# Kernel tuning notes

Hardware: AMD Instinct MI355X
Metric: run time of the kernel (lower is better)

The kernel has to match this reference:

```python
import jax, jax.numpy as jnp
import numpy as np

BS, DIM, EMB_DIM, SRC, TDEC, NEMB = 64, 512, 512, 400, 100, 50257


def intra_attention(h_t, h, W_attn):
    # h_t: [bs, dim]; h: [n, bs, dim]; W_attn: [dim, dim]
    n, bs, dim = h.shape
    # Faithful to torch .view([bs, dim, n]) on a contiguous [n, bs, dim]
    # tensor: raw row-major memory reinterpretation (NOT a transpose).
    hv = jnp.reshape(h, (bs, dim, n))  # [bs, dim, n]
    # E_t = (h_t @ W) [bs,1,dim] bmm hv [bs,dim,n] -> [bs, n]
    E = jnp.einsum('bd,bdn->bn', h_t @ W_attn, hv)
    # sum-normalized (non-softmax) score, eq. (4)
    A = E / jnp.sum(E, axis=1, keepdims=True)  # [bs, n]
    C = jnp.einsum('bdn,bn->bd', hv, A)        # [bs, dim]
    return A, C


def pointer_generator(ae_t, ce_t, hd_t, cd_t, W_emb, W_proj, W_u, b_u, b_out):
    # c_cat: [3*dim, bs]
    c_cat = jnp.concatenate((hd_t, ce_t, cd_t), axis=1).T
    # p_switch: [bs]
    p_switch = jax.nn.sigmoid(W_u @ c_cat + b_u).squeeze(0)
    # shared-embedding output projection, sect 2.4
    W_out = jnp.tanh(W_emb @ W_proj)           # [n_emb, 3*dim]
    logits = W_out @ c_cat + b_out             # [n_emb, bs]
    p_vocab = jax.nn.softmax(logits, axis=0)   # softmax over vocab
    p_gen = ((1.0 - p_switch) * p_vocab).T     # [bs, n_emb]
    p_copy = p_switch[:, None] * ae_t          # [bs, src]
    return p_gen, p_copy


def setup_inputs() -> dict:
    key = jax.random.key(0)
    ks = jax.random.split(key, 12)
    inp = {
        'h_t': jax.random.uniform(ks[0], (BS, DIM), dtype=jnp.float32),
        'h_enc': jax.random.uniform(ks[1], (SRC, BS, DIM), dtype=jnp.float32),
        'h_dec': jax.random.uniform(ks[2], (TDEC, BS, DIM), dtype=jnp.float32),
        'x': jax.random.randint(ks[3], (SRC, BS, 1), 0, NEMB, dtype=jnp.int64) if jax.config.jax_enable_x64 else jax.random.randint(ks[3], (SRC, BS, 1), 0, NEMB, dtype=jnp.int32),
        # positive attention weights keep the sum-normalized score well-conditioned
        'W_attn_enc': jax.random.uniform(ks[4], (DIM, DIM), dtype=jnp.float32, maxval=0.05),
        'W_attn_dec': jax.random.uniform(ks[5], (DIM, DIM), dtype=jnp.float32, maxval=0.05),
        'W_emb': jax.random.normal(ks[6], (NEMB, EMB_DIM), dtype=jnp.float32) * 0.02,
        'W_proj': jax.random.normal(ks[7], (EMB_DIM, 3 * DIM), dtype=jnp.float32) * 0.02,
        'W_u': jax.random.normal(ks[8], (1, 3 * DIM), dtype=jnp.float32) * 0.02,
        'b_u': jnp.zeros((1,), dtype=jnp.float32),
        'b_out': jnp.zeros((NEMB, 1), dtype=jnp.float32),
    }
    return inp


def reference(h_t, h_enc, h_dec, x, W_attn_enc, W_attn_dec, W_emb, W_proj, W_u, b_u, b_out):
    # one decode step of ReinforcedDecoder: enc attn + dec attn + pointer-gen
    ae_t, ce_t = intra_attention(h_t, h_enc, W_attn_enc)
    ad_t, cd_t = intra_attention(h_t, h_dec, W_attn_dec)
    p_gen, p_copy = pointer_generator(ae_t, ce_t, h_t, cd_t,
                                      W_emb, W_proj, W_u, b_u, b_out)
    return p_gen, p_copy
```

## Files before the change

kernel.cpp:

```cpp
#include <hip/hip_runtime.h>
#include <math.h>

typedef __attribute__((ext_vector_type(8))) short bf16x8;
typedef __attribute__((ext_vector_type(4))) float f32x4;
typedef __attribute__((ext_vector_type(4))) float f4v;

#define BS   64
#define DIM  512
#define SRC  400
#define TDEC 100
#define NEMB 50257
#define K3   1536

#define WS_Q     0
#define WS_EENC  65536
#define WS_EDEC  91136
#define WS_CENC  97536
#define WS_CDEC  130304
#define WS_ESUM  163072
#define WS_PSW   163200
#define WS_SMAX  163264
#define WS_SSUM  163328
#define WS_WPT   163392
#define WS_CCB   556608
#define WS_ZBEG  WS_CENC
#define WS_ZCNT  (WS_WPT - WS_CENC)

__device__ __forceinline__ ushort f2bf(float x) {
    union { float f; unsigned u; } v; v.f = x;
    unsigned r = (v.u + 0x7FFFu + ((v.u >> 16) & 1u)) >> 16;
    return (ushort)r;
}
__device__ __forceinline__ bf16x8 pack8v(f4v a, f4v b) {
    union { ushort us[8]; bf16x8 v; } p;
    p.us[0] = f2bf(a.x); p.us[1] = f2bf(a.y); p.us[2] = f2bf(a.z); p.us[3] = f2bf(a.w);
    p.us[4] = f2bf(b.x); p.us[5] = f2bf(b.y); p.us[6] = f2bf(b.z); p.us[7] = f2bf(b.w);
    return p.v;
}
__device__ __forceinline__ float pade_tanh(float x) {
    const float x2 = x * x;
    const float num = x * fmaf(x2, 1.0f / 15.0f, 1.0f);
    const float den = fmaf(x2, 0.4f, 1.0f);
    return num * __frcp_rn(den);
}
__device__ __forceinline__ unsigned fenc(float f) {
    unsigned b = __float_as_uint(f);
    return (b & 0x80000000u) ? ~b : (b | 0x80000000u);
}
__device__ __forceinline__ float fdec(unsigned k) {
    unsigned b = (k & 0x80000000u) ? (k & 0x7FFFFFFFu) : ~k;
    return __uint_as_float(b);
}
__device__ __forceinline__ void gl2lds16(const void* g, void* l) {
    __builtin_amdgcn_global_load_lds(
        (const __attribute__((address_space(1))) unsigned int*)g,
        (__attribute__((address_space(3))) unsigned int*)l, 16, 0, 0);
}

__global__ __launch_bounds__(256) void k_prep(const float* __restrict__ h_t,
                                              const float* __restrict__ Wenc,
                                              const float* __restrict__ Wdec,
                                              const float* __restrict__ Wp,
                                              float* __restrict__ ws) {
    const int tid = threadIdx.x;
    if (blockIdx.x < 32) {
        __shared__ float sh[64 * 65 + 64 * 33];
        const int which = blockIdx.x >> 4;
        const int c0 = (blockIdx.x & 15) * 32;
        const float* W = which ? Wdec : Wenc;
        float* q = ws + WS_Q + which * (BS * DIM);
        float* hS = sh;
        float* WSm = sh + 64 * 65;
        const int c = tid & 31, bg = tid >> 5;
        float acc[8] = {0.f, 0.f, 0.f, 0.f, 0.f, 0.f, 0.f, 0.f};
        for (int kc = 0; kc < 8; ++kc) {
            __syncthreads();
            #pragma unroll
            for (int r = 0; r < 16; ++r) {
                const int idx = r * 256 + tid;
                const int b = idx >> 6, k = idx & 63;
                hS[b * 65 + k] = h_t[b * DIM + kc * 64 + k];
            }
            #pragma unroll
            for (int r = 0; r < 8; ++r) {
                const int idx = r * 256 + tid;
                const int k = idx >> 5, cc = idx & 31;
                WSm[k * 33 + cc] = W[(size_t)(kc * 64 + k) * DIM + c0 + cc];
            }
            __syncthreads();
            #pragma unroll 8
            for (int k = 0; k < 64; ++k) {
                const float wv = WSm[k * 33 + c];
                #pragma unroll
                for (int bb = 0; bb < 8; ++bb)
                    acc[bb] = fmaf(hS[(bg * 8 + bb) * 65 + k], wv, acc[bb]);
            }
        }
        #pragma unroll
        for (int bb = 0; bb < 8; ++bb)
            q[(bg * 8 + bb) * DIM + c0 + c] = acc[bb];
    } else {
        __shared__ float T32[64][132];
        const int bid = blockIdx.x - 32;
        const int t = bid >> 2, kh = (bid >> 1) & 1, khalf = bid & 1;
        const int kbase = kh * 256 + khalf * 128;
        const int jbase = t * 64;
        const int kk = tid >> 4, jj4 = (tid & 15) * 4;
        #pragma unroll
        for (int p = 0; p < 8; ++p) {
            const int kl = kk + p * 16;
            const float4 v = *(const float4*)(Wp + (size_t)(kbase + kl) * K3 + jbase + jj4);
            T32[jj4 + 0][kl] = v.x; T32[jj4 + 1][kl] = v.y;
            T32[jj4 + 2][kl] = v.z; T32[jj4 + 3][kl] = v.w;
        }
        __syncthreads();
        char* dst = (char*)(ws + WS_WPT) + (size_t)(t * 2 + kh) * 32768;
        #pragma unroll
        for (int it = 0; it < 4; ++it) {
            const int idx = it * 256 + tid;
            const int j = idx >> 4;
            const int kc8 = (idx & 15) * 8;
            const f4v a = *(const f4v*)&T32[j][kc8];
            const f4v b = *(const f4v*)&T32[j][kc8 + 4];
            const int kb = (khalf * 256 + kc8 * 2) ^ ((j & 7) << 4);
            *(bf16x8*)(dst + j * 512 + kb) = pack8v(a, b);
        }
    }
}

#define IC 16
__global__ __launch_bounds__(256) void k_attn(const float* __restrict__ h_enc,
                                              const float* __restrict__ h_dec,
                                              float* __restrict__ ws) {
    const int b = blockIdx.x, which = blockIdx.y, z = blockIdx.z;
    const int tid = threadIdx.x;
    const int n   = which ? TDEC : SRC;
    const int per = which ? (TDEC / 4) : (SRC / 4);
    const int i_begin = z * per, i_end = i_begin + per;
    const float* h  = which ? h_dec : h_enc;
    const float* q  = ws + WS_Q + which * (BS * DIM) + b * DIM;
    float* wsE      = ws + (which ? WS_EDEC : WS_EENC) + b * n;
    float* Cws      = ws + (which ? WS_CDEC : WS_CENC) + b * DIM;
    const float* hb = h + (size_t)b * DIM * n;

    __shared__ float hS[DIM * (IC + 1)];
    __shared__ float qs[DIM];
    __shared__ float Ered[256];
    __shared__ float Es[IC];

    qs[tid] = q[tid];
    qs[tid + 256] = q[tid + 256];

    const int ii = tid & (IC - 1);
    const int dg = tid >> 4;
    float c0 = 0.f, c1 = 0.f, esum = 0.f;

    for (int i0 = i_begin; i0 < i_end; i0 += IC) {
        const int ic = min(IC, i_end - i0);
        __syncthreads();
        #pragma unroll 8
        for (int idx = tid; idx < DIM * IC; idx += 256) {
            const int d = idx >> 4, i = idx & (IC - 1);
            hS[d * (IC + 1) + i] = (i < ic) ? hb[(size_t)d * n + i0 + i] : 0.f;
        }
        __syncthreads();
        float p = 0.f;
        #pragma unroll 8
        for (int d = dg * 32; d < dg * 32 + 32; ++d) p += qs[d] * hS[d * (IC + 1) + ii];
        Ered[dg * IC + ii] = p;
        __syncthreads();
        if (tid < IC) {
            float e = 0.f;
            #pragma unroll
            for (int g = 0; g < 16; ++g) e += Ered[g * IC + tid];
            Es[tid] = e;
            esum += e;
            if (tid < ic) wsE[i0 + tid] = e;
        }
        __syncthreads();
        #pragma unroll
        for (int i = 0; i < IC; ++i) {
            const float e = Es[i];
            c0 += hS[tid * (IC + 1) + i] * e;
            c1 += hS[(tid + 256) * (IC + 1) + i] * e;
        }
    }
    atomicAdd(&Cws[tid], c0);
    atomicAdd(&Cws[tid + 256], c1);
    __syncthreads();
    if (tid < IC) Ered[tid] = esum;
    __syncthreads();
    if (tid == 0) {
        float s = 0.f;
        #pragma unroll
        for (int g = 0; g < IC; ++g) s += Ered[g];
        atomicAdd(&ws[WS_ESUM + which * 64 + b], s);
    }
}

__global__ void k_pswitch(const float* __restrict__ h_t,
                          const float* __restrict__ W_u,
                          const float* __restrict__ b_u,
                          float* __restrict__ out_copy,
                          float* __restrict__ ws) {
    const int b = blockIdx.x, tid = threadIdx.x;
    const float invE = 1.f / ws[WS_ESUM + b];
    const float invD = 1.f / ws[WS_ESUM + 64 + b];
    const float* Ce = ws + WS_CENC + b * DIM;
    const float* Cd = ws + WS_CDEC + b * DIM;
    ushort* ccB = (ushort*)(ws + WS_CCB);
    __shared__ float red[256];
    float part = 0.f;
    #pragma unroll
    for (int r = 0; r < 6; ++r) {
        const int j = tid + r * 256;
        float v = (j < DIM) ? h_t[b * DIM + j]
                            : ((j < 2 * DIM) ? Ce[j - DIM] * invE : Cd[j - 2 * DIM] * invD);
        ccB[(size_t)b * K3 + j] = f2bf(v);
        part += W_u[j] * v;
    }
    red[tid] = part;
    __syncthreads();
    for (int s = 128; s > 0; s >>= 1) {
        if (tid < s) red[tid] += red[tid + s];
        __syncthreads();
    }
    const float ps = 1.f / (1.f + expf(-(red[0] + b_u[0])));
    if (tid == 0) ws[WS_PSW + b] = ps;
    const float* Ee = ws + WS_EENC + b * SRC;
    for (int i = tid; i < SRC; i += 256) out_copy[b * SRC + i] = ps * Ee[i] * invE;
}

#define VB 64
#define GEMM1(BUF, F0)                                                          \
    {                                                                           \
        _Pragma("unroll")                                                       \
        for (int ks = 0; ks < 8; ++ks) {                                        \
            const int kb = (ks * 64 + lgrp * 16) ^ swz;                         \
            const char* bp = (BUF) + lrow * 512 + kb;                           \
            const bf16x8 b0 = *(const bf16x8*)(bp);                             \
            const bf16x8 b1 = *(const bf16x8*)(bp + 8192);                      \
            const bf16x8 b2 = *(const bf16x8*)(bp + 16384);                     \
            const bf16x8 b3 = *(const bf16x8*)(bp + 24576);                     \
            Ta[0] = __builtin_amdgcn_mfma_f32_16x16x32_bf16(A[(F0) + ks], b0, Ta[0], 0, 0, 0); \
            Ta[1] = __builtin_amdgcn_mfma_f32_16x16x32_bf16(A[(F0) + ks], b1, Ta[1], 0, 0, 0); \
            Ta[2] = __builtin_amdgcn_mfma_f32_16x16x32_bf16(A[(F0) + ks], b2, Ta[2], 0, 0, 0); \
            Ta[3] = __builtin_amdgcn_mfma_f32_16x16x32_bf16(A[(F0) + ks], b3, Ta[3], 0, 0, 0); \
        }                                                                       \
    }

__global__ __launch_bounds__(256, 2) void k_bigmm(const float* __restrict__ We,
                                                  const float* __restrict__ ws,
                                                  const float* __restrict__ b_out,
                                                  float* __restrict__ out) {
    __shared__ __align__(16) char smem[65536];
    const ushort* ccB = (const ushort*)(ws + WS_CCB);
    const char* wptb  = (const char*)(ws + WS_WPT);

    const int tid  = threadIdx.x;
    const int w    = tid >> 6, lane = tid & 63;
    const int lrow = lane & 15, lgrp = lane >> 4;
    const int vw   = blockIdx.x * VB + w * 16;
    const int row  = vw + lrow;
    char* B0 = smem;
    char* B1 = smem + 32768;
    char* tbase = B1 + w * 2048;
    const int swz = (lrow & 7) << 4;

    {
        const char* src = wptb + (size_t)w * 8192 + lane * 16;
        char* dst = B0 + w * 8192;
        #pragma unroll
        for (int c = 0; c < 8; ++c) gl2lds16(src + c * 1024, dst + c * 1024);
    }

    bf16x8 A[16];
    if (row < NEMB) {
        const f4v* p = (const f4v*)(We + (size_t)row * DIM + lgrp * 8);
        #pragma unroll
        for (int f = 0; f < 16; ++f) {
            const f4v x0 = __builtin_nontemporal_load(p + f * 8);
            const f4v x1 = __builtin_nontemporal_load(p + f * 8 + 1);
            A[f] = pack8v(x0, x1);
        }
    } else {
        #pragma unroll
        for (int f = 0; f < 16; ++f) A[f] = (bf16x8){0, 0, 0, 0, 0, 0, 0, 0};
    }

    f32x4 La[4];
    #pragma unroll
    for (int i = 0; i < 4; ++i) La[i] = (f32x4){0.f, 0.f, 0.f, 0.f};

    __syncthreads();

    for (int t = 0; t < 24; ++t) {
        {
            const char* src = wptb + (size_t)(t * 2 + 1) * 32768 + w * 8192 + lane * 16;
            char* dst = B1 + w * 8192;
            #pragma unroll
            for (int c = 0; c < 8; ++c) gl2lds16(src + c * 1024, dst + c * 1024);
        }
        f32x4 Ta[4];
        #pragma unroll
        for (int i = 0; i < 4; ++i) Ta[i] = (f32x4){0.f, 0.f, 0.f, 0.f};
        GEMM1(B0, 0);
        __syncthreads();

        if (t < 23) {
            const char* src = wptb + (size_t)(t + 1) * 65536 + w * 8192 + lane * 16;
            char* dst = B0 + w * 8192;
            #pragma unroll
            for (int c = 0; c < 8; ++c) gl2lds16(src + c * 1024, dst + c * 1024);
        }
        GEMM1(B1, 8);
        __syncthreads();

        #pragma unroll
        for (int nj = 0; nj < 4; ++nj) {
            const int j = nj * 16 + lrow;
            #pragma unroll
            for (int r = 0; r < 4; ++r) {
                const int v = lgrp * 4 + r;
                *(ushort*)(tbase + v * 128 + ((j * 2) ^ ((v & 7) << 4))) =
                    f2bf(pade_tanh(Ta[nj][r]));
            }
        }
        #pragma unroll
        for (int kc = 0; kc < 2; ++kc) {
            const bf16x8 tf = *(const bf16x8*)(tbase + lrow * 128 +
                                               ((kc * 64 + lgrp * 16) ^ swz));
            const ushort* cc = ccB + (size_t)lrow * K3 + t * 64 + kc * 32 + lgrp * 8;
            const bf16x8 c0 = *(const bf16x8*)(cc);
            const bf16x8 c1 = *(const bf16x8*)(cc + 16 * K3);
            const bf16x8 c2 = *(const bf16x8*)(cc + 32 * K3);
            const bf16x8 c3 = *(const bf16x8*)(cc + 48 * K3);
            La[0] = __builtin_amdgcn_mfma_f32_16x16x32_bf16(tf, c0, La[0], 0, 0, 0);
            La[1] = __builtin_amdgcn_mfma_f32_16x16x32_bf16(tf, c1, La[1], 0, 0, 0);
            La[2] = __builtin_amdgcn_mfma_f32_16x16x32_bf16(tf, c2, La[2], 0, 0, 0);
            La[3] = __builtin_amdgcn_mfma_f32_16x16x32_bf16(tf, c3, La[3], 0, 0, 0);
        }
        __syncthreads();
    }

    #pragma unroll
    for (int nb = 0; nb < 4; ++nb) {
        const int b = nb * 16 + lrow;
        #pragma unroll
        for (int r = 0; r < 4; ++r) {
            const int v = vw + lgrp * 4 + r;
            if (v < NEMB) out[(size_t)b * NEMB + v] = La[nb][r] + b_out[v];
        }
    }
}

#define VC 12565
__global__ void k_colmax(const float* __restrict__ out, float* __restrict__ ws) {
    const int b = blockIdx.x, vc = blockIdx.y, tid = threadIdx.x;
    const float* L = out + (size_t)b * NEMB;
    const int vend = min((vc + 1) * VC, NEMB);
    float m = -1e30f;
    for (int v = vc * VC + tid; v < vend; v += 256) m = fmaxf(m, L[v]);
    __shared__ float red[256];
    red[tid] = m;
    __syncthreads();
    for (int s = 128; s > 0; s >>= 1) {
        if (tid < s) red[tid] = fmaxf(red[tid], red[tid + s]);
        __syncthreads();
    }
    if (tid == 0) atomicMax((unsigned*)(ws + WS_SMAX) + b, fenc(red[0]));
}

__global__ void k_colsum(const float* __restrict__ out, float* __restrict__ ws) {
    const int b = blockIdx.x, vc = blockIdx.y, tid = threadIdx.x;
    const float* L = out + (size_t)b * NEMB;
    const float mb = fdec(((const unsigned*)(ws + WS_SMAX))[b]);
    const int vend = min((vc + 1) * VC, NEMB);
    float sum = 0.f;
    for (int v = vc * VC + tid; v < vend; v += 256) sum += expf(L[v] - mb);
    __shared__ float red[256];
    red[tid] = sum;
    __syncthreads();
    for (int s = 128; s > 0; s >>= 1) {
        if (tid < s) red[tid] += red[tid + s];
        __syncthreads();
    }
    if (tid == 0) atomicAdd(ws + WS_SSUM + b, red[0]);
}

__global__ void k_finalize(float* __restrict__ out, const float* __restrict__ ws) {
    const int total = BS * NEMB;
    const int stride = gridDim.x * blockDim.x;
    for (int idx = blockIdx.x * blockDim.x + threadIdx.x; idx < total; idx += stride) {
        const int b = idx / NEMB;
        const float mb = fdec(((const unsigned*)(ws + WS_SMAX))[b]);
        const float sb = ws[WS_SSUM + b];
        const float ps = ws[WS_PSW + b];
        out[idx] = (1.f - ps) * expf(out[idx] - mb) / sb;
    }
}

extern "C" void kernel_launch(void* const* d_in, const int* in_sizes, int n_in,
                              void* d_out, int out_size, void* d_ws, size_t ws_size,
                              hipStream_t stream) {
    const float* h_t        = (const float*)d_in[0];
    const float* h_enc      = (const float*)d_in[1];
    const float* h_dec      = (const float*)d_in[2];
    const float* W_attn_enc = (const float*)d_in[4];
    const float* W_attn_dec = (const float*)d_in[5];
    const float* W_emb      = (const float*)d_in[6];
    const float* W_proj     = (const float*)d_in[7];
    const float* W_u        = (const float*)d_in[8];
    const float* b_u        = (const float*)d_in[9];
    const float* b_out      = (const float*)d_in[10];

    float* out = (float*)d_out;
    float* ws  = (float*)d_ws;
    float* out_copy = out + (size_t)BS * NEMB;

    hipMemsetAsync(ws + WS_ZBEG, 0, (size_t)WS_ZCNT * sizeof(float), stream);
    k_prep   <<<128, 256, 0, stream>>>(h_t, W_attn_enc, W_attn_dec, W_proj, ws);
    k_attn   <<<dim3(64, 2, 4), 256, 0, stream>>>(h_enc, h_dec, ws);
    k_pswitch<<<64, 256, 0, stream>>>(h_t, W_u, b_u, out_copy, ws);
    k_bigmm  <<<(NEMB + VB - 1) / VB, 256, 0, stream>>>(W_emb, ws, b_out, out);
    k_colmax <<<dim3(64, 4), 256, 0, stream>>>(out, ws);
    k_colsum <<<dim3(64, 4), 256, 0, stream>>>(out, ws);
    k_finalize<<<4096, 256, 0, stream>>>(out, ws);
}
```

Baseline: 363.3 us.

## Shrink bigmm LDS staging to 16KB chunks and pre-fragment W_proj layout for occupancy 4

The prep kernel now writes the transposed bf16 W_proj in MFMA-fragment order, in 16KB chunks, so each lane reads its B operand with a plain linear 16-byte LDS load and no swizzle. The bigmm kernel drops from a 64KB to a 40KB LDS footprint with double-buffered 16KB chunks, and launch bounds rise from 2 to 4 blocks per CU to raise occupancy and hide latency. The cost is four barriers per 64-column tile instead of three, smaller prefetch granularity, and a tighter register budget that could cause spills given the 16-fragment A array kept in registers.

```diff
diff --git a/kernel.cpp b/kernel.cpp
--- a/kernel.cpp
+++ b/kernel.cpp
@@ -62,9 +62,9 @@
                                               const float* __restrict__ Wdec,
                                               const float* __restrict__ Wp,
                                               float* __restrict__ ws) {
+    __shared__ float sh[128 * 68];
     const int tid = threadIdx.x;
     if (blockIdx.x < 32) {
-        __shared__ float sh[64 * 65 + 64 * 33];
         const int which = blockIdx.x >> 4;
         const int c0 = (blockIdx.x & 15) * 32;
         const float* W = which ? Wdec : Wenc;
@@ -100,30 +100,33 @@
         for (int bb = 0; bb < 8; ++bb)
             q[(bg * 8 + bb) * DIM + c0 + c] = acc[bb];
     } else {
-        __shared__ float T32[64][132];
         const int bid = blockIdx.x - 32;
-        const int t = bid >> 2, kh = (bid >> 1) & 1, khalf = bid & 1;
-        const int kbase = kh * 256 + khalf * 128;
-        const int jbase = t * 64;
-        const int kk = tid >> 4, jj4 = (tid & 15) * 4;
+        const int t = bid >> 2, c = bid & 3;
+        float (*T32)[68] = (float (*)[68])sh;
         #pragma unroll
         for (int p = 0; p < 8; ++p) {
-            const int kl = kk + p * 16;
-            const float4 v = *(const float4*)(Wp + (size_t)(kbase + kl) * K3 + jbase + jj4);
-            T32[jj4 + 0][kl] = v.x; T32[jj4 + 1][kl] = v.y;
-            T32[jj4 + 2][kl] = v.z; T32[jj4 + 3][kl] = v.w;
-        }
-        __syncthreads();
-        char* dst = (char*)(ws + WS_WPT) + (size_t)(t * 2 + kh) * 32768;
-        #pragma unroll
-        for (int it = 0; it < 4; ++it) {
-            const int idx = it * 256 + tid;
-            const int j = idx >> 4;
-            const int kc8 = (idx & 15) * 8;
-            const f4v a = *(const f4v*)&T32[j][kc8];
-            const f4v b = *(const f4v*)&T32[j][kc8 + 4];
-            const int kb = (khalf * 256 + kc8 * 2) ^ ((j & 7) << 4);
-            *(bf16x8*)(dst + j * 512 + kb) = pack8v(a, b);
+            const int idx = p * 256 + tid;
+            const int kk = idx >> 4, s = idx & 15;
+            const float4 v = *(const float4*)(Wp + (size_t)(c * 128 + kk) * K3 + t * 64 + s * 4);
+            T32[kk][s * 4 + 0] = v.x; T32[kk][s * 4 + 1] = v.y;
+            T32[kk][s * 4 + 2] = v.z; T32[kk][s * 4 + 3] = v.w;
+        }
+        __syncthreads();
+        char* dst = (char*)(ws + WS_WPT) + (size_t)bid * 16384;
+        #pragma unroll
+        for (int p = 0; p < 4; ++p) {
+            const int fid = p * 256 + tid;
+            const int lane = fid & 63;
+            const int J = (fid >> 6) & 3;
+            const int ks = fid >> 8;
+            const int j = J * 16 + (lane & 15);
+            const int k0 = ks * 32 + (lane >> 4) * 8;
+            f4v a, b;
+            a.x = T32[k0 + 0][j]; a.y = T32[k0 + 1][j];
+            a.z = T32[k0 + 2][j]; a.w = T32[k0 + 3][j];
+            b.x = T32[k0 + 4][j]; b.y = T32[k0 + 5][j];
+            b.z = T32[k0 + 6][j]; b.w = T32[k0 + 7][j];
+            *(bf16x8*)(dst + fid * 16) = pack8v(a, b);
         }
     }
 }
@@ -232,28 +235,11 @@
 }
 
 #define VB 64
-#define GEMM1(BUF, F0)                                                          \
-    {                                                                           \
-        _Pragma("unroll")                                                       \
-        for (int ks = 0; ks < 8; ++ks) {                                        \
-            const int kb = (ks * 64 + lgrp * 16) ^ swz;                         \
-            const char* bp = (BUF) + lrow * 512 + kb;                           \
-            const bf16x8 b0 = *(const bf16x8*)(bp);                             \
-            const bf16x8 b1 = *(const bf16x8*)(bp + 8192);                      \
-            const bf16x8 b2 = *(const bf16x8*)(bp + 16384);                     \
-            const bf16x8 b3 = *(const bf16x8*)(bp + 24576);                     \
-            Ta[0] = __builtin_amdgcn_mfma_f32_16x16x32_bf16(A[(F0) + ks], b0, Ta[0], 0, 0, 0); \
-            Ta[1] = __builtin_amdgcn_mfma_f32_16x16x32_bf16(A[(F0) + ks], b1, Ta[1], 0, 0, 0); \
-            Ta[2] = __builtin_amdgcn_mfma_f32_16x16x32_bf16(A[(F0) + ks], b2, Ta[2], 0, 0, 0); \
-            Ta[3] = __builtin_amdgcn_mfma_f32_16x16x32_bf16(A[(F0) + ks], b3, Ta[3], 0, 0, 0); \
-        }                                                                       \
-    }
-
-__global__ __launch_bounds__(256, 2) void k_bigmm(const float* __restrict__ We,
+__global__ __launch_bounds__(256, 4) void k_bigmm(const float* __restrict__ We,
                                                   const float* __restrict__ ws,
                                                   const float* __restrict__ b_out,
                                                   float* __restrict__ out) {
-    __shared__ __align__(16) char smem[65536];
+    __shared__ __align__(16) char smem[40960];
     const ushort* ccB = (const ushort*)(ws + WS_CCB);
     const char* wptb  = (const char*)(ws + WS_WPT);
 
@@ -262,16 +248,14 @@
     const int lrow = lane & 15, lgrp = lane >> 4;
     const int vw   = blockIdx.x * VB + w * 16;
     const int row  = vw + lrow;
-    char* B0 = smem;
-    char* B1 = smem + 32768;
-    char* tbase = B1 + w * 2048;
+    char* tbase = smem + 32768 + w * 2048;
     const int swz = (lrow & 7) << 4;
 
     {
-        const char* src = wptb + (size_t)w * 8192 + lane * 16;
-        char* dst = B0 + w * 8192;
-        #pragma unroll
-        for (int c = 0; c < 8; ++c) gl2lds16(src + c * 1024, dst + c * 1024);
+        const char* src = wptb + tid * 16;
+        char* dst = smem + tid * 16;
+        #pragma unroll
+        for (int rnd = 0; rnd < 4; ++rnd) gl2lds16(src + rnd * 4096, dst + rnd * 4096);
     }
 
     bf16x8 A[16];
@@ -288,59 +272,70 @@
         for (int f = 0; f < 16; ++f) A[f] = (bf16x8){0, 0, 0, 0, 0, 0, 0, 0};
     }
 
-    f32x4 La[4];
+    f32x4 La[4], Ta[4];
     #pragma unroll
-    for (int i = 0; i < 4; ++i) La[i] = (f32x4){0.f, 0.f, 0.f, 0.f};
+    for (int i = 0; i < 4; ++i) {
+        La[i] = (f32x4){0.f, 0.f, 0.f, 0.f};
+        Ta[i] = (f32x4){0.f, 0.f, 0.f, 0.f};
+    }
 
     __syncthreads();
 
     for (int t = 0; t < 24; ++t) {
-        {
-            const char* src = wptb + (size_t)(t * 2 + 1) * 32768 + w * 8192 + lane * 16;
-            char* dst = B1 + w * 8192;
-            #pragma unroll
-            for (int c = 0; c < 8; ++c) gl2lds16(src + c * 1024, dst + c * 1024);
-        }
-        f32x4 Ta[4];
-        #pragma unroll
-        for (int i = 0; i < 4; ++i) Ta[i] = (f32x4){0.f, 0.f, 0.f, 0.f};
-        GEMM1(B0, 0);
-        __syncthreads();
-
-        if (t < 23) {
-            const char* src = wptb + (size_t)(t + 1) * 65536 + w * 8192 + lane * 16;
-            char* dst = B0 + w * 8192;
-            #pragma unroll
-            for (int c = 0; c < 8; ++c) gl2lds16(src + c * 1024, dst + c * 1024);
-        }
-        GEMM1(B1, 8);
-        __syncthreads();
-
-        #pragma unroll
-        for (int nj = 0; nj < 4; ++nj) {
-            const int j = nj * 16 + lrow;
-            #pragma unroll
-            for (int r = 0; r < 4; ++r) {
-                const int v = lgrp * 4 + r;
-                *(ushort*)(tbase + v * 128 + ((j * 2) ^ ((v & 7) << 4))) =
-                    f2bf(pade_tanh(Ta[nj][r]));
-            }
-        }
-        #pragma unroll
-        for (int kc = 0; kc < 2; ++kc) {
-            const bf16x8 tf = *(const bf16x8*)(tbase + lrow * 128 +
-                                               ((kc * 64 + lgrp * 16) ^ swz));
-            const ushort* cc = ccB + (size_t)lrow * K3 + t * 64 + kc * 32 + lgrp * 8;
-            const bf16x8 c0 = *(const bf16x8*)(cc);
-            const bf16x8 c1 = *(const bf16x8*)(cc + 16 * K3);
-            const bf16x8 c2 = *(const bf16x8*)(cc + 32 * K3);
-            const bf16x8 c3 = *(const bf16x8*)(cc + 48 * K3);
-            La[0] = __builtin_amdgcn_mfma_f32_16x16x32_bf16(tf, c0, La[0], 0, 0, 0);
-            La[1] = __builtin_amdgcn_mfma_f32_16x16x32_bf16(tf, c1, La[1], 0, 0, 0);
-            La[2] = __builtin_amdgcn_mfma_f32_16x16x32_bf16(tf, c2, La[2], 0, 0, 0);
-            La[3] = __builtin_amdgcn_mfma_f32_16x16x32_bf16(tf, c3, La[3], 0, 0, 0);
-        }
-        __syncthreads();
+        #pragma unroll
+        for (int c = 0; c < 4; ++c) {
+            const int nxt = t * 4 + c + 1;
+            if (nxt < 96) {
+                const char* src = wptb + (size_t)nxt * 16384 + tid * 16;
+                char* dst = smem + ((c & 1) ^ 1) * 16384 + tid * 16;
+                #pragma unroll
+                for (int rnd = 0; rnd < 4; ++rnd)
+                    gl2lds16(src + rnd * 4096, dst + rnd * 4096);
+            }
+            {
+                const char* bp = smem + (c & 1) * 16384 + lane * 16;
+                #pragma unroll
+                for (int ks = 0; ks < 4; ++ks) {
+                    const bf16x8 b0 = *(const bf16x8*)(bp + ks * 4096);
+                    const bf16x8 b1 = *(const bf16x8*)(bp + ks * 4096 + 1024);
+                    const bf16x8 b2 = *(const bf16x8*)(bp + ks * 4096 + 2048);
+                    const bf16x8 b3 = *(const bf16x8*)(bp + ks * 4096 + 3072);
+                    Ta[0] = __builtin_amdgcn_mfma_f32_16x16x32_bf16(A[c * 4 + ks], b0, Ta[0], 0, 0, 0);
+                    Ta[1] = __builtin_amdgcn_mfma_f32_16x16x32_bf16(A[c * 4 + ks], b1, Ta[1], 0, 0, 0);
+                    Ta[2] = __builtin_amdgcn_mfma_f32_16x16x32_bf16(A[c * 4 + ks], b2, Ta[2], 0, 0, 0);
+                    Ta[3] = __builtin_amdgcn_mfma_f32_16x16x32_bf16(A[c * 4 + ks], b3, Ta[3], 0, 0, 0);
+                }
+            }
+            if (c == 3) {
+                #pragma unroll
+                for (int nj = 0; nj < 4; ++nj) {
+                    const int j = nj * 16 + lrow;
+                    #pragma unroll
+                    for (int r = 0; r < 4; ++r) {
+                        const int v = lgrp * 4 + r;
+                        *(ushort*)(tbase + v * 128 + ((j * 2) ^ ((v & 7) << 4))) =
+                            f2bf(pade_tanh(Ta[nj][r]));
+                    }
+                }
+                #pragma unroll
+                for (int kc = 0; kc < 2; ++kc) {
+                    const bf16x8 tf = *(const bf16x8*)(tbase + lrow * 128 +
+                                                       ((kc * 64 + lgrp * 16) ^ swz));
+                    const ushort* cc = ccB + (size_t)lrow * K3 + t * 64 + kc * 32 + lgrp * 8;
+                    const bf16x8 c0 = *(const bf16x8*)(cc);
+                    const bf16x8 c1 = *(const bf16x8*)(cc + 16 * K3);
+                    const bf16x8 c2 = *(const bf16x8*)(cc + 32 * K3);
+                    const bf16x8 c3 = *(const bf16x8*)(cc + 48 * K3);
+                    La[0] = __builtin_amdgcn_mfma_f32_16x16x32_bf16(tf, c0, La[0], 0, 0, 0);
+                    La[1] = __builtin_amdgcn_mfma_f32_16x16x32_bf16(tf, c1, La[1], 0, 0, 0);
+                    La[2] = __builtin_amdgcn_mfma_f32_16x16x32_bf16(tf, c2, La[2], 0, 0, 0);
+                    La[3] = __builtin_amdgcn_mfma_f32_16x16x32_bf16(tf, c3, La[3], 0, 0, 0);
+                }
+                #pragma unroll
+                for (int i = 0; i < 4; ++i) Ta[i] = (f32x4){0.f, 0.f, 0.f, 0.f};
+            }
+            __syncthreads();
+        }
     }
 
     #pragma unroll
```

Result: slower. 398.8 us (+9.8%).
